# Kernel optimization log

Hardware: AMD Instinct MI355X
Metric: run time of the kernel (lower is better)

Reference implementation:

```python
import jax, jax.numpy as jnp
import numpy as np

NUM_HEADS = 4
GROUPS = 8
EPS = 1e-5


def group_norm(x, w, b):
    B, C, H, W = x.shape
    xg = x.reshape(B, GROUPS, C // GROUPS, H, W)
    mu = jnp.mean(xg, axis=(2, 3, 4), keepdims=True)
    var = jnp.var(xg, axis=(2, 3, 4), keepdims=True)
    xg = (xg - mu) * jax.lax.rsqrt(var + EPS)
    x = xg.reshape(B, C, H, W)
    return x * w[None, :, None, None] + b[None, :, None, None]


def setup_inputs() -> dict:
    key = jax.random.key(0)
    k1, k2, k3 = jax.random.split(key, 3)
    B, C, H, W = 16, 256, 32, 32
    x = jax.random.normal(k1, (B, C, H, W), dtype=jnp.float32)
    gn_w = jnp.ones((C,), dtype=jnp.float32)
    gn_b = jnp.zeros((C,), dtype=jnp.float32)
    qkv_w = jax.random.normal(k2, (3 * C, C), dtype=jnp.float32) * 0.02
    qkv_b = jnp.zeros((3 * C,), dtype=jnp.float32)
    proj_w = jax.random.normal(k3, (C, C), dtype=jnp.float32) * 0.02
    proj_b = jnp.zeros((C,), dtype=jnp.float32)
    return {"x": x, "gn_w": gn_w, "gn_b": gn_b, "qkv_w": qkv_w,
            "qkv_b": qkv_b, "proj_w": proj_w, "proj_b": proj_b}


def reference(x, gn_w, gn_b, qkv_w, qkv_b, proj_w, proj_b):
    B, C, H, W = x.shape
    Dh = C // NUM_HEADS
    N = H * W
    skip = x
    xn = group_norm(x, gn_w, gn_b)
    # 1x1 conv QKV projection: [B,3C,H,W]
    qkv = jnp.einsum('oc,bchw->bohw', qkv_w, xn) + qkv_b[None, :, None, None]
    # split channel dim 3C -> [3, heads, Dh], flatten spatial -> N
    qkv = qkv.reshape(B, 3, NUM_HEADS, Dh, N)
    qkv = jnp.transpose(qkv, (1, 0, 2, 4, 3))  # [3,B,heads,N,Dh]
    q, k, v = qkv[0], qkv[1], qkv[2]
    scale = 1.0 / np.sqrt(Dh).astype(np.float32)
    attn = jnp.einsum('bhnd,bhmd->bhnm', q, k) * scale  # [B,heads,N,N]
    attn = jax.nn.softmax(attn, axis=-1)
    out = jnp.einsum('bhnm,bhmd->bhnd', attn, v)  # [B,heads,N,Dh]
    out = jnp.transpose(out, (0, 1, 3, 2)).reshape(B, C, H, W)
    out = jnp.einsum('oc,bchw->bohw', proj_w, out) + proj_b[None, :, None, None]
    return out + skip
```

## Files before the change

kernel.cpp:

```cpp
#include <hip/hip_runtime.h>

typedef unsigned short u16;
typedef __bf16 bf16x8 __attribute__((ext_vector_type(8)));
typedef float f32x4 __attribute__((ext_vector_type(4)));

#define QSCALE 0.18033688011112042f

__device__ __forceinline__ u16 f2bf(float f) {
  __bf16 h = (__bf16)f;
  union { __bf16 b; u16 u; } cv;
  cv.b = h;
  return cv.u;
}
__device__ __forceinline__ unsigned pack2(float a, float b) {
#if __has_builtin(__builtin_amdgcn_cvt_pk_bf16_f32)
  typedef __bf16 bf16x2 __attribute__((ext_vector_type(2)));
  bf16x2 p = __builtin_amdgcn_cvt_pk_bf16_f32(a, b);
  union { bf16x2 v; unsigned u; } cv;
  cv.v = p;
  return cv.u;
#else
  return (unsigned)f2bf(a) | ((unsigned)f2bf(b) << 16);
#endif
}
__device__ __forceinline__ float fexp2(float x) {
  return __builtin_amdgcn_exp2f(x);
}

__global__ __launch_bounds__(256) void prep(
    const float* __restrict__ qw, const float* __restrict__ pw,
    const float* __restrict__ x,
    u16* __restrict__ qwb, u16* __restrict__ pwb, float* __restrict__ stats) {
  __shared__ float sh1[256], sh2[256];
  const int blk = blockIdx.x;
  const int t = threadIdx.x;
  if (blk < 256) {
    int i = blk * 256 + t;
    const float* s; u16* d; int j;
    if (i < 49152) { s = qw; d = qwb; j = i; }
    else           { s = pw; d = pwb; j = i - 49152; }
    float4 v = *(const float4*)(s + (size_t)j * 4);
    uint2 o; o.x = pack2(v.x, v.y); o.y = pack2(v.z, v.w);
    *(uint2*)(d + (size_t)j * 4) = o;
    return;
  }
  const int bid = blk - 256;
  int cl = t >> 3;
  int off = (t & 7) * 4;
  const float* p = x + (size_t)bid * 32768 + (size_t)cl * 1024 + off;
  float s = 0.f, ss = 0.f;
#pragma unroll 8
  for (int i = 0; i < 32; ++i) {
    float4 v = *(const float4*)(p + i * 32);
    s += v.x + v.y + v.z + v.w;
    ss += v.x * v.x + v.y * v.y + v.z * v.z + v.w * v.w;
  }
  sh1[t] = s; sh2[t] = ss;
  __syncthreads();
  for (int st = 128; st > 0; st >>= 1) {
    if (t < st) { sh1[t] += sh1[t + st]; sh2[t] += sh2[t + st]; }
    __syncthreads();
  }
  if (t == 0) {
    float mean = sh1[0] * (1.f / 32768.f);
    float var = sh2[0] * (1.f / 32768.f) - mean * mean;
    stats[bid * 2] = mean;
    stats[bid * 2 + 1] = rsqrtf(var + 1e-5f);
  }
}

__global__ __launch_bounds__(256) void gemm_qkv(
    const u16* __restrict__ A, const float* __restrict__ x,
    const float* __restrict__ stats,
    const float* __restrict__ gw, const float* __restrict__ gb,
    const float* __restrict__ bias,
    u16* __restrict__ o_q, u16* __restrict__ o_k, u16* __restrict__ o_v) {
  const int l = blockIdx.x;
  const int xcd = l & 7;
  const int i2 = l >> 3;
  const int m_t = i2 % 6;
  const int nl6 = i2 / 6;
  const int nt = xcd * 16 + nl6;
  const int m0 = m_t * 128;
  const int n0 = nt * 128;
  const int b = nt >> 3;
  const int nsp0 = (nt & 7) * 128;

  const int t = threadIdx.x;
  const int wave = t >> 6, lane = t & 63, lm = lane & 15, quad = lane >> 4;
  const int wr = wave >> 1, wc = wave & 1;

  __shared__ u16 As[2][128 * 32];
  __shared__ u16 Bs[2][128 * 32];

  f32x4 acc[4][4];
  const f32x4 fzero = {0.f, 0.f, 0.f, 0.f};
#pragma unroll
  for (int i = 0; i < 4; ++i)
#pragma unroll
    for (int j = 0; j < 4; ++j) acc[i][j] = fzero;

  const int srow = t >> 2, scol = (t & 3) * 8;
  const u16* pA0 = A + (size_t)(m0 + srow) * 256 + scol;
  const u16* pA1 = A + (size_t)(m0 + 64 + srow) * 256 + scol;

  const int n2 = t & 63, gq = t >> 6;
  const float* xb = x + (size_t)b * 262144 + nsp0 + 2 * n2;
  const int gsw = (gq ^ (n2 & 3)) * 8;

  float2 vB[8];
  uint4 vA0, vA1;

#define LD_B(ki)                                                       \
  {                                                                    \
    const int cb = (ki) * 32 + gq * 8;                                 \
    _Pragma("unroll") for (int i = 0; i < 8; ++i)                      \
        vB[i] = *(const float2*)(xb + (size_t)(cb + i) * 1024);        \
  }
#define ST_B(ki, buf)                                                  \
  {                                                                    \
    const int cb = (ki) * 32 + gq * 8;                                 \
    const float mu = stats[(b * 8 + (ki)) * 2];                        \
    const float rq = stats[(b * 8 + (ki)) * 2 + 1];                    \
    float e0[8], e1[8];                                                \
    _Pragma("unroll") for (int i = 0; i < 8; ++i) {                    \
      const float w = gw[cb + i] * rq;                                 \
      const float bb = gb[cb + i] - mu * w;                            \
      e0[i] = vB[i].x * w + bb;                                        \
      e1[i] = vB[i].y * w + bb;                                        \
    }                                                                  \
    uint4 w0, w1;                                                      \
    w0.x = pack2(e0[0], e0[1]); w0.y = pack2(e0[2], e0[3]);            \
    w0.z = pack2(e0[4], e0[5]); w0.w = pack2(e0[6], e0[7]);            \
    w1.x = pack2(e1[0], e1[1]); w1.y = pack2(e1[2], e1[3]);            \
    w1.z = pack2(e1[4], e1[5]); w1.w = pack2(e1[6], e1[7]);            \
    *(uint4*)(Bs[buf] + (2 * n2) * 32 + gsw) = w0;                     \
    *(uint4*)(Bs[buf] + (2 * n2 + 1) * 32 + gsw) = w1;                 \
  }

  LD_B(0);
  vA0 = *(const uint4*)pA0;
  vA1 = *(const uint4*)pA1;
  ST_B(0, 0);
  *(uint4*)(As[0] + srow * 32 + scol) = vA0;
  *(uint4*)(As[0] + (64 + srow) * 32 + scol) = vA1;
  LD_B(1);
  vA0 = *(const uint4*)(pA0 + 32);
  vA1 = *(const uint4*)(pA1 + 32);

  for (int ki = 0; ki < 8; ++ki) {
    __syncthreads();
    if (ki + 1 < 8) {
      ST_B(ki + 1, (ki + 1) & 1);
      u16* as = As[(ki + 1) & 1];
      *(uint4*)(as + srow * 32 + scol) = vA0;
      *(uint4*)(as + (64 + srow) * 32 + scol) = vA1;
    }
    if (ki + 2 < 8) {
      LD_B(ki + 2);
      vA0 = *(const uint4*)(pA0 + (ki + 2) * 32);
      vA1 = *(const uint4*)(pA1 + (ki + 2) * 32);
    }
    const u16* as = As[ki & 1];
    const u16* bs = Bs[ki & 1];
    bf16x8 af[4], bf[4];
#pragma unroll
    for (int mb = 0; mb < 4; ++mb)
      af[mb] = *(const bf16x8*)(as + (wr * 64 + mb * 16 + lm) * 32 + quad * 8);
#pragma unroll
    for (int nb = 0; nb < 4; ++nb) {
      const int row = wc * 64 + nb * 16 + lm;
      bf[nb] = *(const bf16x8*)(bs + row * 32 + ((quad ^ ((row >> 1) & 3)) * 8));
    }
#pragma unroll
    for (int mb = 0; mb < 4; ++mb)
#pragma unroll
      for (int nb = 0; nb < 4; ++nb)
        acc[mb][nb] = __builtin_amdgcn_mfma_f32_16x16x32_bf16(af[mb], bf[nb],
                                                              acc[mb][nb], 0, 0, 0);
  }
#undef LD_B
#undef ST_B

#pragma unroll
  for (int mb = 0; mb < 4; ++mb) {
#pragma unroll
    for (int nb = 0; nb < 4; ++nb) {
      const int o = m0 + wr * 64 + mb * 16 + 4 * quad;
      const int ng = n0 + wc * 64 + nb * 16 + lm;
      const int bb = ng >> 10, n = ng & 1023;
      const int kind = o >> 8;
      if (kind == 1) {
        ushort4 pk;
        pk.x = f2bf(acc[mb][nb][0] + bias[o]);
        pk.y = f2bf(acc[mb][nb][1] + bias[o + 1]);
        pk.z = f2bf(acc[mb][nb][2] + bias[o + 2]);
        pk.w = f2bf(acc[mb][nb][3] + bias[o + 3]);
        const int h = (o >> 6) & 3;
        *(ushort4*)(o_k + ((size_t)((bb * 4 + h) * 1024 + n)) * 64 + (o & 63)) = pk;
      } else {
        u16* dst = (kind == 0) ? o_q : o_v;
        const float sc = (kind == 0) ? QSCALE : 1.f;
        const int oc = o & 255;
#pragma unroll
        for (int r = 0; r < 4; ++r)
          dst[((size_t)(bb * 256 + oc + r)) * 1024 + n] =
              f2bf((acc[mb][nb][r] + bias[o + r]) * sc);
      }
    }
  }
}

__global__ __launch_bounds__(256) void gemm_proj(
    const u16* __restrict__ A, const u16* __restrict__ Bm,
    const float* __restrict__ bias,
    const float* __restrict__ skip, float* __restrict__ out) {
  const int m0 = blockIdx.y * 64;
  const int n0 = blockIdx.x * 128;
  const int t = threadIdx.x;
  const int wave = t >> 6, lane = t & 63, lm = lane & 15, quad = lane >> 4;
  const int wr = wave >> 1, wc = wave & 1;

  __shared__ u16 As[2][64 * 32];
  __shared__ u16 Bs[2][128 * 32];

  f32x4 acc[2][4];
  const f32x4 fzero = {0.f, 0.f, 0.f, 0.f};
#pragma unroll
  for (int i = 0; i < 2; ++i)
#pragma unroll
    for (int j = 0; j < 4; ++j) acc[i][j] = fzero;

  const int srow = t >> 2, scol = (t & 3) * 8;
  const u16* pA0 = A + (size_t)(m0 + srow) * 256 + scol;
  const u16* pB0 = Bm + (size_t)(n0 + srow) * 256 + scol;
  const u16* pB1 = Bm + (size_t)(n0 + 64 + srow) * 256 + scol;

  uint4 pa0 = *(const uint4*)pA0;
  uint4 pb0 = *(const uint4*)pB0;
  uint4 pb1 = *(const uint4*)pB1;
  *(uint4*)(As[0] + srow * 32 + scol) = pa0;
  *(uint4*)(Bs[0] + srow * 32 + scol) = pb0;
  *(uint4*)(Bs[0] + (64 + srow) * 32 + scol) = pb1;
  pa0 = *(const uint4*)(pA0 + 32);
  pb0 = *(const uint4*)(pB0 + 32);
  pb1 = *(const uint4*)(pB1 + 32);

  for (int ki = 0; ki < 8; ++ki) {
    __syncthreads();
    if (ki + 1 < 8) {
      u16* as = As[(ki + 1) & 1];
      u16* bs = Bs[(ki + 1) & 1];
      *(uint4*)(as + srow * 32 + scol) = pa0;
      *(uint4*)(bs + srow * 32 + scol) = pb0;
      *(uint4*)(bs + (64 + srow) * 32 + scol) = pb1;
    }
    if (ki + 2 < 8) {
      const int ko = (ki + 2) * 32;
      pa0 = *(const uint4*)(pA0 + ko);
      pb0 = *(const uint4*)(pB0 + ko);
      pb1 = *(const uint4*)(pB1 + ko);
    }
    const u16* as = As[ki & 1];
    const u16* bs = Bs[ki & 1];
    bf16x8 af[2], bf[4];
#pragma unroll
    for (int mb = 0; mb < 2; ++mb)
      af[mb] = *(const bf16x8*)(as + (wr * 32 + mb * 16 + lm) * 32 + quad * 8);
#pragma unroll
    for (int nb = 0; nb < 4; ++nb)
      bf[nb] = *(const bf16x8*)(bs + (wc * 64 + nb * 16 + lm) * 32 + quad * 8);
#pragma unroll
    for (int mb = 0; mb < 2; ++mb)
#pragma unroll
      for (int nb = 0; nb < 4; ++nb)
        acc[mb][nb] = __builtin_amdgcn_mfma_f32_16x16x32_bf16(af[mb], bf[nb],
                                                              acc[mb][nb], 0, 0, 0);
  }

#pragma unroll
  for (int mb = 0; mb < 2; ++mb) {
#pragma unroll
    for (int nb = 0; nb < 4; ++nb) {
      const int o = m0 + wr * 32 + mb * 16 + 4 * quad;
      const int ng = n0 + wc * 64 + nb * 16 + lm;
      const int b = ng >> 10, n = ng & 1023;
#pragma unroll
      for (int r = 0; r < 4; ++r) {
        const size_t oi = ((size_t)(b * 256 + o + r)) * 1024 + n;
        out[oi] = acc[mb][nb][r] + bias[o + r] + skip[oi];
      }
    }
  }
}

__global__ __launch_bounds__(256) void attn_fused(
    const u16* __restrict__ qdn, const u16* __restrict__ knd,
    const u16* __restrict__ vdn, u16* __restrict__ att) {
  const int bid = blockIdx.x;
  const int bh = (bid & 7) * 8 + ((bid >> 3) & 7);
  const int qtile = bid >> 6;
  const int t = threadIdx.x;
  const int wave = t >> 6, lane = t & 63, lm = lane & 15, quad = lane >> 4;

  const u16* qb = qdn + (size_t)bh * 65536;
  const u16* kb = knd + (size_t)bh * 65536;
  const u16* vb = vdn + (size_t)bh * 65536;

  __shared__ u16 KV[2][2][64 * 64];
  __shared__ u16 QP[64 * 64];

  const int e1 = t + 256;
  const int r0 = t >> 3, c0_ = t & 7, r1 = e1 >> 3, c1_ = e1 & 7;
  const int lk0 = r0 * 64 + ((c0_ ^ (r0 & 7)) * 8);
  const int lk1 = r1 * 64 + ((c1_ ^ (r1 & 7)) * 8);
  const u16* kg0 = kb + r0 * 64 + c0_ * 8;
  const u16* kg1 = kb + r1 * 64 + c1_ * 8;
  const u16* vg0 = vb + r0 * 1024 + c0_ * 8;
  const u16* vg1 = vb + r1 * 1024 + c1_ * 8;

  uint4 pk0 = *(const uint4*)kg0;
  uint4 pk1 = *(const uint4*)kg1;
  uint4 pv0 = *(const uint4*)vg0;
  uint4 pv1 = *(const uint4*)vg1;

  {
    union { uint4 v; u16 s[8]; } tq0, tq1;
    const int d0 = t >> 3, ngq = t & 7;
    tq0.v = *(const uint4*)(qb + (size_t)d0 * 1024 + qtile * 64 + ngq * 8);
    tq1.v = *(const uint4*)(qb + (size_t)(32 + d0) * 1024 + qtile * 64 + ngq * 8);
    const int oa = d0 >> 3, ob = 4 + oa, dl = d0 & 7;
#pragma unroll
    for (int k = 0; k < 8; ++k) {
      const int row = ngq * 8 + k;
      QP[row * 64 + ((oa ^ k) * 8) + dl] = tq0.s[k];
      QP[row * 64 + ((ob ^ k) * 8) + dl] = tq1.s[k];
    }
  }

  *(uint4*)(KV[0][0] + lk0) = pk0;
  *(uint4*)(KV[0][0] + lk1) = pk1;
  *(uint4*)(KV[0][1] + lk0) = pv0;
  *(uint4*)(KV[0][1] + lk1) = pv1;
  pk0 = *(const uint4*)(kg0 + 4096);
  pk1 = *(const uint4*)(kg1 + 4096);
  pv0 = *(const uint4*)(vg0 + 64);
  pv1 = *(const uint4*)(vg1 + 64);
  __syncthreads();

  const int swz0 = (quad ^ (lm & 7)) * 8;
  const int swz1 = ((4 + quad) ^ (lm & 7)) * 8;
  u16* Pw = QP + (wave * 16 + lm) * 64;
  const bf16x8 qf0 = *(const bf16x8*)(Pw + swz0);
  const bf16x8 qf1 = *(const bf16x8*)(Pw + swz1);

  const f32x4 fzero = {0.f, 0.f, 0.f, 0.f};
  f32x4 oacc[4];
#pragma unroll
  for (int d = 0; d < 4; ++d) oacc[d] = fzero;
  float lp = 0.f;

  for (int jc = 0; jc < 16; ++jc) {
    if (jc) __syncthreads();
    if (jc + 1 < 16) {
      u16* kd = KV[(jc + 1) & 1][0];
      u16* vd = KV[(jc + 1) & 1][1];
      *(uint4*)(kd + lk0) = pk0;
      *(uint4*)(kd + lk1) = pk1;
      *(uint4*)(vd + lk0) = pv0;
      *(uint4*)(vd + lk1) = pv1;
    }
    if (jc + 2 < 16) {
      pk0 = *(const uint4*)(kg0 + (jc + 2) * 4096);
      pk1 = *(const uint4*)(kg1 + (jc + 2) * 4096);
      pv0 = *(const uint4*)(vg0 + (jc + 2) * 64);
      pv1 = *(const uint4*)(vg1 + (jc + 2) * 64);
    }
    const u16* Ks = KV[jc & 1][0];
    const u16* Vs = KV[jc & 1][1];

    f32x4 sacc[4];
#pragma unroll
    for (int jb = 0; jb < 4; ++jb) sacc[jb] = fzero;
#pragma unroll
    for (int jb = 0; jb < 4; ++jb) {
      const int row = (jb * 16 + lm) * 64;
      bf16x8 kf0 = *(const bf16x8*)(Ks + row + swz0);
      bf16x8 kf1 = *(const bf16x8*)(Ks + row + swz1);
      sacc[jb] = __builtin_amdgcn_mfma_f32_16x16x32_bf16(kf0, qf0, sacc[jb], 0, 0, 0);
      sacc[jb] = __builtin_amdgcn_mfma_f32_16x16x32_bf16(kf1, qf1, sacc[jb], 0, 0, 0);
    }
#pragma unroll
    for (int jb = 0; jb < 4; ++jb) {
      const float e0 = fexp2(sacc[jb][0]);
      const float e1_ = fexp2(sacc[jb][1]);
      const float e2 = fexp2(sacc[jb][2]);
      const float e3 = fexp2(sacc[jb][3]);
      lp += (e0 + e1_) + (e2 + e3);
      uint2 pw;
      pw.x = pack2(e0, e1_);
      pw.y = pack2(e2, e3);
      const int oct = 2 * jb + (quad >> 1);
      *(uint2*)(Pw + ((oct ^ (lm & 7)) * 8) + 4 * (quad & 1)) = pw;
    }
    bf16x8 pf0 = *(const bf16x8*)(Pw + swz0);
    bf16x8 pf1 = *(const bf16x8*)(Pw + swz1);
#pragma unroll
    for (int db = 0; db < 4; ++db) {
      const int row = (db * 16 + lm) * 64;
      bf16x8 vf0 = *(const bf16x8*)(Vs + row + swz0);
      bf16x8 vf1 = *(const bf16x8*)(Vs + row + swz1);
      oacc[db] = __builtin_amdgcn_mfma_f32_16x16x32_bf16(pf0, vf0, oacc[db], 0, 0, 0);
      oacc[db] = __builtin_amdgcn_mfma_f32_16x16x32_bf16(pf1, vf1, oacc[db], 0, 0, 0);
    }
  }

  float rs = lp;
  rs += __shfl_xor(rs, 16);
  rs += __shfl_xor(rs, 32);
  const int b = bh >> 2, h = bh & 3;
#pragma unroll
  for (int r = 0; r < 4; ++r) {
    const float inv = 1.f / __shfl(rs, 4 * quad + r);
    const int n = qtile * 64 + wave * 16 + 4 * quad + r;
#pragma unroll
    for (int db = 0; db < 4; ++db) {
      const int c = h * 64 + db * 16 + lm;
      att[((size_t)(b * 1024 + n)) * 256 + c] = f2bf(oacc[db][r] * inv);
    }
  }
}

extern "C" void kernel_launch(void* const* d_in, const int* in_sizes, int n_in,
                              void* d_out, int out_size, void* d_ws, size_t ws_size,
                              hipStream_t stream) {
  const float* x      = (const float*)d_in[0];
  const float* gn_w   = (const float*)d_in[1];
  const float* gn_b   = (const float*)d_in[2];
  const float* qkv_w  = (const float*)d_in[3];
  const float* qkv_b  = (const float*)d_in[4];
  const float* proj_w = (const float*)d_in[5];
  const float* proj_b = (const float*)d_in[6];
  float* out = (float*)d_out;

  char* ws = (char*)d_ws;
  float* stats = (float*)(ws + 0);
  u16* qwb = (u16*)(ws + 4096);
  u16* pwb = (u16*)(ws + 397312);
  u16* qdn = (u16*)(ws + 8916992);
  u16* knd = (u16*)(ws + 17305600);
  u16* vdn = (u16*)(ws + 25694208);
  u16* att = (u16*)(ws + 34082816);

  prep<<<384, 256, 0, stream>>>(qkv_w, proj_w, x, qwb, pwb, stats);
  gemm_qkv<<<768, 256, 0, stream>>>(qwb, x, stats, gn_w, gn_b, qkv_b,
                                    qdn, knd, vdn);
  attn_fused<<<1024, 256, 0, stream>>>(qdn, knd, vdn, att);
  gemm_proj<<<dim3(128, 4), 256, 0, stream>>>(pwb, att, proj_b, x, out);
}
```

Before: 140.0 us.

## Pre-swizzle Q/K/V in GEMM epilogue and stream tiles via direct global-to-LDS loads

The QKV GEMM epilogue now writes Q, K and V in tile-contiguous, XOR-swizzled layouts that match the attention kernel's shared-memory layout. The attention kernel can then copy each 64x64 tile straight into LDS with global_load_lds 16-byte copies. This removes the register staging, the per-element Q transpose scatter and the prefetch registers. The cost is more scattered, smaller stores in the GEMM epilogue (V is written element by element into a transposed swizzle). Correctness now depends on the async LDS loads being complete before the existing __syncthreads.

After: 138.9 us. About the same (-0.8%).

```diff
diff --git a/kernel.cpp b/kernel.cpp
--- a/kernel.cpp
+++ b/kernel.cpp
@@ -25,6 +25,11 @@
 }
 __device__ __forceinline__ float fexp2(float x) {
   return __builtin_amdgcn_exp2f(x);
+}
+__device__ __forceinline__ void cp16(const u16* g, u16* l) {
+  __builtin_amdgcn_global_load_lds(
+      (const __attribute__((address_space(1))) void*)g,
+      (__attribute__((address_space(3))) void*)l, 16, 0, 0);
 }
 
 __global__ __launch_bounds__(256) void prep(
@@ -190,22 +195,28 @@
       const int ng = n0 + wc * 64 + nb * 16 + lm;
       const int bb = ng >> 10, n = ng & 1023;
       const int kind = o >> 8;
-      if (kind == 1) {
-        ushort4 pk;
-        pk.x = f2bf(acc[mb][nb][0] + bias[o]);
-        pk.y = f2bf(acc[mb][nb][1] + bias[o + 1]);
-        pk.z = f2bf(acc[mb][nb][2] + bias[o + 2]);
-        pk.w = f2bf(acc[mb][nb][3] + bias[o + 3]);
-        const int h = (o >> 6) & 3;
-        *(ushort4*)(o_k + ((size_t)((bb * 4 + h) * 1024 + n)) * 64 + (o & 63)) = pk;
+      const int h = (o >> 6) & 3;
+      const int dd = o & 63;
+      const int jc = n >> 6, jl = n & 63;
+      const size_t bhoff = ((size_t)(bb * 4 + h)) * 65536 + jc * 4096;
+      if (kind <= 1) {
+        const float sc = (kind == 0) ? QSCALE : 1.f;
+        u16* base = (kind == 0) ? o_q : o_k;
+        ushort4 pq;
+        pq.x = f2bf((acc[mb][nb][0] + bias[o]) * sc);
+        pq.y = f2bf((acc[mb][nb][1] + bias[o + 1]) * sc);
+        pq.z = f2bf((acc[mb][nb][2] + bias[o + 2]) * sc);
+        pq.w = f2bf((acc[mb][nb][3] + bias[o + 3]) * sc);
+        *(ushort4*)(base + bhoff + jl * 64 + (((dd >> 3) ^ (jl & 7)) * 8) +
+                    (dd & 7)) = pq;
       } else {
-        u16* dst = (kind == 0) ? o_q : o_v;
-        const float sc = (kind == 0) ? QSCALE : 1.f;
-        const int oc = o & 255;
-#pragma unroll
-        for (int r = 0; r < 4; ++r)
-          dst[((size_t)(bb * 256 + oc + r)) * 1024 + n] =
-              f2bf((acc[mb][nb][r] + bias[o + r]) * sc);
+        u16* vbase = o_v + bhoff + (jl & 7);
+#pragma unroll
+        for (int r = 0; r < 4; ++r) {
+          const int d = dd + r;
+          vbase[d * 64 + (((jl >> 3) ^ (d & 7)) * 8)] =
+              f2bf(acc[mb][nb][r] + bias[o + r]);
+        }
       }
     }
   }
@@ -295,57 +306,29 @@
 }
 
 __global__ __launch_bounds__(256) void attn_fused(
-    const u16* __restrict__ qdn, const u16* __restrict__ knd,
-    const u16* __restrict__ vdn, u16* __restrict__ att) {
+    const u16* __restrict__ qsw, const u16* __restrict__ ksw,
+    const u16* __restrict__ vsw, u16* __restrict__ att) {
   const int bid = blockIdx.x;
   const int bh = (bid & 7) * 8 + ((bid >> 3) & 7);
   const int qtile = bid >> 6;
   const int t = threadIdx.x;
   const int wave = t >> 6, lane = t & 63, lm = lane & 15, quad = lane >> 4;
 
-  const u16* qb = qdn + (size_t)bh * 65536;
-  const u16* kb = knd + (size_t)bh * 65536;
-  const u16* vb = vdn + (size_t)bh * 65536;
-
-  __shared__ u16 KV[2][2][64 * 64];
-  __shared__ u16 QP[64 * 64];
-
-  const int e1 = t + 256;
-  const int r0 = t >> 3, c0_ = t & 7, r1 = e1 >> 3, c1_ = e1 & 7;
-  const int lk0 = r0 * 64 + ((c0_ ^ (r0 & 7)) * 8);
-  const int lk1 = r1 * 64 + ((c1_ ^ (r1 & 7)) * 8);
-  const u16* kg0 = kb + r0 * 64 + c0_ * 8;
-  const u16* kg1 = kb + r1 * 64 + c1_ * 8;
-  const u16* vg0 = vb + r0 * 1024 + c0_ * 8;
-  const u16* vg1 = vb + r1 * 1024 + c1_ * 8;
-
-  uint4 pk0 = *(const uint4*)kg0;
-  uint4 pk1 = *(const uint4*)kg1;
-  uint4 pv0 = *(const uint4*)vg0;
-  uint4 pv1 = *(const uint4*)vg1;
-
-  {
-    union { uint4 v; u16 s[8]; } tq0, tq1;
-    const int d0 = t >> 3, ngq = t & 7;
-    tq0.v = *(const uint4*)(qb + (size_t)d0 * 1024 + qtile * 64 + ngq * 8);
-    tq1.v = *(const uint4*)(qb + (size_t)(32 + d0) * 1024 + qtile * 64 + ngq * 8);
-    const int oa = d0 >> 3, ob = 4 + oa, dl = d0 & 7;
-#pragma unroll
-    for (int k = 0; k < 8; ++k) {
-      const int row = ngq * 8 + k;
-      QP[row * 64 + ((oa ^ k) * 8) + dl] = tq0.s[k];
-      QP[row * 64 + ((ob ^ k) * 8) + dl] = tq1.s[k];
-    }
-  }
-
-  *(uint4*)(KV[0][0] + lk0) = pk0;
-  *(uint4*)(KV[0][0] + lk1) = pk1;
-  *(uint4*)(KV[0][1] + lk0) = pv0;
-  *(uint4*)(KV[0][1] + lk1) = pv1;
-  pk0 = *(const uint4*)(kg0 + 4096);
-  pk1 = *(const uint4*)(kg1 + 4096);
-  pv0 = *(const uint4*)(vg0 + 64);
-  pv1 = *(const uint4*)(vg1 + 64);
+  const u16* qb = qsw + (size_t)bh * 65536 + qtile * 4096;
+  const u16* kb = ksw + (size_t)bh * 65536;
+  const u16* vb = vsw + (size_t)bh * 65536;
+
+  __shared__ u16 KV[2][2][4096];
+  __shared__ u16 QP[4096];
+
+  const int t8 = t * 8;
+
+  cp16(qb + t8, QP + t8);
+  cp16(qb + 2048 + t8, QP + 2048 + t8);
+  cp16(kb + t8, KV[0][0] + t8);
+  cp16(kb + 2048 + t8, KV[0][0] + 2048 + t8);
+  cp16(vb + t8, KV[0][1] + t8);
+  cp16(vb + 2048 + t8, KV[0][1] + 2048 + t8);
   __syncthreads();
 
   const int swz0 = (quad ^ (lm & 7)) * 8;
@@ -363,18 +346,13 @@
   for (int jc = 0; jc < 16; ++jc) {
     if (jc) __syncthreads();
     if (jc + 1 < 16) {
+      const int base = (jc + 1) * 4096;
       u16* kd = KV[(jc + 1) & 1][0];
       u16* vd = KV[(jc + 1) & 1][1];
-      *(uint4*)(kd + lk0) = pk0;
-      *(uint4*)(kd + lk1) = pk1;
-      *(uint4*)(vd + lk0) = pv0;
-      *(uint4*)(vd + lk1) = pv1;
-    }
-    if (jc + 2 < 16) {
-      pk0 = *(const uint4*)(kg0 + (jc + 2) * 4096);
-      pk1 = *(const uint4*)(kg1 + (jc + 2) * 4096);
-      pv0 = *(const uint4*)(vg0 + (jc + 2) * 64);
-      pv1 = *(const uint4*)(vg1 + (jc + 2) * 64);
+      cp16(kb + base + t8, kd + t8);
+      cp16(kb + base + 2048 + t8, kd + 2048 + t8);
+      cp16(vb + base + t8, vd + t8);
+      cp16(vb + base + 2048 + t8, vd + 2048 + t8);
     }
     const u16* Ks = KV[jc & 1][0];
     const u16* Vs = KV[jc & 1][1];
@@ -447,14 +425,14 @@
   float* stats = (float*)(ws + 0);
   u16* qwb = (u16*)(ws + 4096);
   u16* pwb = (u16*)(ws + 397312);
-  u16* qdn = (u16*)(ws + 8916992);
-  u16* knd = (u16*)(ws + 17305600);
-  u16* vdn = (u16*)(ws + 25694208);
+  u16* qsw = (u16*)(ws + 8916992);
+  u16* ksw = (u16*)(ws + 17305600);
+  u16* vsw = (u16*)(ws + 25694208);
   u16* att = (u16*)(ws + 34082816);
 
   prep<<<384, 256, 0, stream>>>(qkv_w, proj_w, x, qwb, pwb, stats);
   gemm_qkv<<<768, 256, 0, stream>>>(qwb, x, stats, gn_w, gn_b, qkv_b,
-                                    qdn, knd, vdn);
-  attn_fused<<<1024, 256, 0, stream>>>(qdn, knd, vdn, att);
+                                    qsw, ksw, vsw);
+  attn_fused<<<1024, 256, 0, stream>>>(qsw, ksw, vsw, att);
   gemm_proj<<<dim3(128, 4), 256, 0, stream>>>(pwb, att, proj_b, x, out);
 }
```
